# Kernel optimization log

Measured on AMD Instinct MI355X. Metric: run time of the kernel, lower is better.

## Reference

```python
import jax, jax.numpy as jnp
import numpy as np


def _conv(x, w, pad):
    # NCHW conv, stride 1
    return jax.lax.conv_general_dilated(
        x, w, window_strides=(1, 1), padding=pad,
        dimension_numbers=('NCHW', 'OIHW', 'NCHW'))


def setup_inputs() -> dict:
    key = jax.random.key(0)
    ks = jax.random.split(key, 8)
    N, Cin, H, W = 8, 512, 64, 64
    Cout, scale = 128, 2
    sd = 0.02
    return {
        'x':     jax.random.normal(ks[0], (N, Cin, H, W), jnp.float32),
        'w_du':  jax.random.normal(ks[1], (Cout, Cin, 3, 1), jnp.float32) * sd,
        'b_du':  jnp.zeros((Cout,), jnp.float32),
        'w_lr':  jax.random.normal(ks[2], (Cout, Cin, 1, 3), jnp.float32) * sd,
        'b_lr':  jnp.zeros((Cout,), jnp.float32),
        'w_1x1': jax.random.normal(ks[3], (Cout, Cin, 1, 1), jnp.float32) * sd,
        'w_ch':  jax.random.normal(ks[4], (Cout, 3 * Cout, 1, 1), jnp.float32) * sd,
        'w_w':   jax.random.normal(ks[5], (Cout * scale, Cout, 1, 1), jnp.float32) * sd,
        'w_H':   jax.random.normal(ks[6], (Cout * scale, Cout, 1, 1), jnp.float32) * sd,
        'scale': scale,
    }


def _conv_du(x, w, b):
    # convDU3, stride=1: the (3,1) conv is applied to each 1-tall row slice with
    # padding (1,0); rows are folded into the batch dim (vectorized, same math).
    N, C, H, W = x.shape
    rows = x.transpose(0, 2, 1, 3).reshape(N * H, C, 1, W)
    y = _conv(rows, w, ((1, 1), (0, 0))) + b[None, :, None, None]
    y = jax.nn.relu(y)                       # (N*H, Cout, 1, W)
    Co = y.shape[1]
    return y.reshape(N, H, Co, W).transpose(0, 2, 1, 3)


def _conv_lr(x, w, b):
    # convLR3, stride=1: (1,3) conv per 1-wide column slice; columns -> batch.
    N, C, H, W = x.shape
    cols = x.transpose(0, 3, 1, 2).reshape(N * W, C, H, 1)
    y = _conv(cols, w, ((0, 0), (1, 1))) + b[None, :, None, None]
    y = jax.nn.relu(y)                       # (N*W, Cout, H, 1)
    Co = y.shape[1]
    return y.reshape(N, W, Co, H).transpose(0, 2, 3, 1)


def reference(x, w_du, b_du, w_lr, b_lr, w_1x1, w_ch, w_w, w_H, scale):
    xdu = _conv_du(x, w_du, b_du)
    xlr = _conv_lr(x, w_lr, b_lr)
    x1 = _conv(x, w_1x1, ((0, 0), (0, 0)))
    x = jnp.concatenate((x1, xlr, xdu), axis=1)
    x = _conv(x, w_ch, ((0, 0), (0, 0)))
    x = _conv(x, w_w, ((0, 0), (0, 0)))      # (N, Cout*scale, H, W)
    N, C, H, W = x.shape
    # height pixel-shuffle: channels -> height
    xp = x.transpose(0, 3, 2, 1).reshape(N, W, H * scale, C // scale)
    xp = xp.transpose(0, 3, 2, 1)            # (N, Cout, H*scale, W)
    xh = _conv(xp, w_H, ((0, 0), (0, 0)))    # (N, Cout*scale, H*scale, W)
    # width pixel-shuffle: channels -> width
    xh = xh.transpose(0, 2, 3, 1).reshape(N, H * scale, W * scale, C // scale)
    return xh.transpose(0, 3, 1, 2)          # (N, Cout, H*scale, W*scale)
```

## Files before the change

### kernel.cpp

```cpp
#include <hip/hip_runtime.h>
#include <hip/hip_bf16.h>
#include <stdint.h>
#include <stddef.h>


typedef __attribute__((ext_vector_type(8))) __bf16 bf16x8;
typedef __attribute__((ext_vector_type(4))) float  f32x4;
typedef __attribute__((ext_vector_type(2))) float  f32x2;
typedef __attribute__((ext_vector_type(4))) unsigned int u32x4;
typedef __attribute__((ext_vector_type(2))) unsigned int u32x2;

#define BAR() asm volatile("s_waitcnt lgkmcnt(0)\n\ts_barrier" ::: "memory")



__global__ __launch_bounds__(256) void prep_k(
    const float* __restrict__ w_ch, const float* __restrict__ w_1x1,
    const float* __restrict__ w_lr, const float* __restrict__ w_du,
    const float* __restrict__ w_H,  const float* __restrict__ w_w,
    __bf16* __restrict__ Wf, __bf16* __restrict__ W2f)
{
  __shared__ float wh[2][128];
  __shared__ float Mrow[2][128];
  int bid = blockIdx.x;
  if (bid < 768) {
    int gid = bid * 256 + threadIdx.x;
    int r = gid >> 9, c = gid & 511;
    float v;
    if (r < 128) {
      const float* a_ = w_ch + r * 384;
      const float* b_ = w_1x1 + c;
      float s0 = 0.f, s1 = 0.f, s2 = 0.f, s3 = 0.f;
      #pragma unroll
      for (int j = 0; j < 128; j += 4) {
        s0 += a_[j + 0] * b_[(size_t)(j + 0) * 512];
        s1 += a_[j + 1] * b_[(size_t)(j + 1) * 512];
        s2 += a_[j + 2] * b_[(size_t)(j + 2) * 512];
        s3 += a_[j + 3] * b_[(size_t)(j + 3) * 512];
      }
      v = (s0 + s1) + (s2 + s3);
    } else if (r < 256) {
      v = w_lr[(r - 128) * 1536 + c * 3 + 1];
    } else {
      v = w_du[(r - 256) * 1536 + c * 3 + 1];
    }
    int gks = c >> 5, lsub = (c >> 3) & 3, jj = c & 7;
    int mfrag = r >> 4, lrow = r & 15;
    Wf[((gks * 24 + mfrag) << 9) + ((lrow + 16 * lsub) << 3) + jj] = (__bf16)v;
  } else {
    int t = threadIdx.x & 127, half = threadIdx.x >> 7;
    int r = (bid - 768) * 2 + half;
    int beta = r >> 8, gam = r & 1, irow = (r >> 1) & 127;
    wh[half][t] = w_H[(gam * 128 + irow) * 128 + t];
    __syncthreads();
    {
      const float* ww = w_w + beta * 16384 + t;
      float s0 = 0.f, s1 = 0.f, s2 = 0.f, s3 = 0.f;
      #pragma unroll
      for (int s = 0; s < 128; s += 4) {
        s0 += wh[half][s + 0] * ww[(s + 0) * 128];
        s1 += wh[half][s + 1] * ww[(s + 1) * 128];
        s2 += wh[half][s + 2] * ww[(s + 2) * 128];
        s3 += wh[half][s + 3] * ww[(s + 3) * 128];
      }
      Mrow[half][t] = (s0 + s1) + (s2 + s3);
    }
    __syncthreads();
    int mfrag = r >> 4, lrow = r & 15;
    #pragma unroll
    for (int c0 = 0; c0 < 384; c0 += 128) {
      int col = c0 + t;
      float v;
      if (c0 == 0) {
        v = Mrow[half][t];
      } else {
        const float* wc = w_ch + col;
        float s0 = 0.f, s1 = 0.f, s2 = 0.f, s3 = 0.f;
        #pragma unroll
        for (int k = 0; k < 128; k += 4) {
          s0 += Mrow[half][k + 0] * wc[(k + 0) * 384];
          s1 += Mrow[half][k + 1] * wc[(k + 1) * 384];
          s2 += Mrow[half][k + 2] * wc[(k + 2) * 384];
          s3 += Mrow[half][k + 3] * wc[(k + 3) * 384];
        }
        v = (s0 + s1) + (s2 + s3);
      }
      int gks = col >> 5, lsub = (col >> 3) & 3, jj = col & 7;
      W2f[((gks * 32 + mfrag) << 9) + ((lrow + 16 * lsub) << 3) + jj] = (__bf16)v;
    }
  }
}


__device__ __forceinline__ int swzB(int px) {
  return (((px & 7) ^ ((px >> 3) & 7)) << 4);
}

__global__ __launch_bounds__(256, 2) void fused_k(
    const float* __restrict__ x, const __bf16* __restrict__ Wf,
    const __bf16* __restrict__ W2f,
    const float* __restrict__ b_lr, const float* __restrict__ b_du,
    float* __restrict__ out)
{
  __shared__ __align__(16) char smem[49152 + 16384];
  char* Tlds = smem;
  char* buf0 = smem + 49152;
  char* buf1 = smem + 49152 + 8192;

  const int tid  = threadIdx.x;
  const int lane = tid & 63;
  const int wv   = tid >> 6;
  const int l15  = lane & 15, lg = lane >> 4;

  const int p0      = blockIdx.x * 64;
  const int img     = p0 >> 12;
  const int pixbase = p0 & 4095;
  const float* xb   = x + (size_t)img * (512 * 4096) + pixbase;
  const char* Wfb   = (const char*)Wf;
  const char* W2b   = (const char*)W2f;

  const int sp4 = (tid & 15) * 4;
  const int sk4 = (tid >> 4) * 4;

  f32x4 ldv[4];
  auto issueS = [&](int kt) {
    #pragma unroll
    for (int j = 0; j < 4; ++j)
      ldv[j] = *(const f32x4*)(xb + (size_t)(kt * 64 + sk4 + j) * 4096 + sp4);
  };
  auto writeS = [&](char* bw) {
    #pragma unroll
    for (int pi = 0; pi < 4; ++pi) {
      int px = sp4 + pi;
      union { __bf16 b[4]; u32x2 u; } wd;
      wd.b[0] = (__bf16)ldv[0][pi];
      wd.b[1] = (__bf16)ldv[1][pi];
      wd.b[2] = (__bf16)ldv[2][pi];
      wd.b[3] = (__bf16)ldv[3][pi];
      *(u32x2*)(bw + px * 128 + ((sk4 * 2) ^ swzB(px))) = wd.u;
    }
  };

  f32x4 acc1[6][4] = {};

  auto compute1 = [&](int kt, const char* bbuf) {
    #pragma unroll
    for (int ks = 0; ks < 2; ++ks) {
      bf16x8 af[6];
      #pragma unroll
      for (int i = 0; i < 6; ++i)
        af[i] = *(const bf16x8*)(Wfb +
            (((kt * 2 + ks) * 24 + wv * 6 + i) << 10) + lane * 16);
      bf16x8 bfr[4];
      #pragma unroll
      for (int j = 0; j < 4; ++j) {
        int rb = j * 16 + l15;
        bfr[j] = *(const bf16x8*)(bbuf + rb * 128 +
                                  ((ks * 64 + lg * 16) ^ swzB(rb)));
      }
      __builtin_amdgcn_s_setprio(1);
      #pragma unroll
      for (int i = 0; i < 6; ++i)
        #pragma unroll
        for (int j = 0; j < 4; ++j)
          acc1[i][j] = __builtin_amdgcn_mfma_f32_16x16x32_bf16(
              af[i], bfr[j], acc1[i][j], 0, 0, 0);
      __builtin_amdgcn_s_setprio(0);
    }
  };

  issueS(0);
  writeS(buf0);
  issueS(1);
  BAR();

  #pragma unroll 1
  for (int kt = 0; kt < 8; ++kt) {
    const char* bcur = (kt & 1) ? buf1 : buf0;
    char* bnext      = (kt & 1) ? buf0 : buf1;
    compute1(kt, bcur);
    if (kt < 7) {
      writeS(bnext);
      if (kt < 6) issueS(kt + 2);
      BAR();
    }
  }

  #pragma unroll
  for (int i = 0; i < 6; ++i) {
    int m0 = wv * 96 + i * 16 + lg * 4;
    bool rl = (m0 >= 128);
    const float* bp = (m0 >= 256) ? (b_du + (m0 - 256)) : (b_lr + (m0 - 128));
    float b0 = 0.f, b1 = 0.f, b2 = 0.f, b3 = 0.f;
    if (rl) { b0 = bp[0]; b1 = bp[1]; b2 = bp[2]; b3 = bp[3]; }
    #pragma unroll
    for (int j = 0; j < 4; ++j) {
      int p = j * 16 + l15;
      union { __bf16 b[4]; u32x2 u; } wd;
      float v0 = acc1[i][j][0], v1 = acc1[i][j][1];
      float v2 = acc1[i][j][2], v3 = acc1[i][j][3];
      if (rl) {
        v0 = fmaxf(v0 + b0, 0.f); v1 = fmaxf(v1 + b1, 0.f);
        v2 = fmaxf(v2 + b2, 0.f); v3 = fmaxf(v3 + b3, 0.f);
      }
      wd.b[0] = (__bf16)v0; wd.b[1] = (__bf16)v1;
      wd.b[2] = (__bf16)v2; wd.b[3] = (__bf16)v3;
      *(u32x2*)(Tlds + p * 768 + ((m0 * 2) ^ ((p & 7) << 4))) = wd.u;
    }
  }
  BAR();

  f32x4 acc2[8][4] = {};
  bf16x8 afA[8], afB[8];
  #pragma unroll
  for (int i = 0; i < 8; ++i)
    afA[i] = *(const bf16x8*)(W2b + ((0 * 32 + wv * 8 + i) << 10) + lane * 16);

  #pragma unroll 1
  for (int g2 = 0; g2 < 6; ++g2) {
    int gA = 2 * g2, gB = 2 * g2 + 1;
    #pragma unroll
    for (int i = 0; i < 8; ++i)
      afB[i] = *(const bf16x8*)(W2b + ((gB * 32 + wv * 8 + i) << 10) + lane * 16);
    {
      bf16x8 bfr[4];
      #pragma unroll
      for (int j = 0; j < 4; ++j) {
        int rb = j * 16 + l15;
        bfr[j] = *(const bf16x8*)(Tlds + rb * 768 +
                                  ((gA * 64 + lg * 16) ^ ((rb & 7) << 4)));
      }
      __builtin_amdgcn_s_setprio(1);
      #pragma unroll
      for (int i = 0; i < 8; ++i)
        #pragma unroll
        for (int j = 0; j < 4; ++j)
          acc2[i][j] = __builtin_amdgcn_mfma_f32_16x16x32_bf16(
              afA[i], bfr[j], acc2[i][j], 0, 0, 0);
      __builtin_amdgcn_s_setprio(0);
    }
    if (g2 < 5) {
      #pragma unroll
      for (int i = 0; i < 8; ++i)
        afA[i] = *(const bf16x8*)(W2b + (((gA + 2) * 32 + wv * 8 + i) << 10) + lane * 16);
    }
    {
      bf16x8 bfr[4];
      #pragma unroll
      for (int j = 0; j < 4; ++j) {
        int rb = j * 16 + l15;
        bfr[j] = *(const bf16x8*)(Tlds + rb * 768 +
                                  ((gB * 64 + lg * 16) ^ ((rb & 7) << 4)));
      }
      __builtin_amdgcn_s_setprio(1);
      #pragma unroll
      for (int i = 0; i < 8; ++i)
        #pragma unroll
        for (int j = 0; j < 4; ++j)
          acc2[i][j] = __builtin_amdgcn_mfma_f32_16x16x32_bf16(
              afB[i], bfr[j], acc2[i][j], 0, 0, 0);
      __builtin_amdgcn_s_setprio(0);
    }
  }

  #pragma unroll
  for (int i = 0; i < 8; ++i) {
    int r = wv * 128 + i * 16 + lg * 4;
    int beta = r >> 8;
    int irow = (r >> 1) & 127;
    #pragma unroll
    for (int j = 0; j < 4; ++j) {
      int pp = pixbase + j * 16 + l15;
      int h = pp >> 6, w = pp & 63;
      size_t o0 = ((((size_t)img * 128 + irow) * 128) + (2 * h + beta)) * 128
                  + 2 * w;
      f32x2 lo; lo.x = acc2[i][j][0]; lo.y = acc2[i][j][1];
      f32x2 hi; hi.x = acc2[i][j][2]; hi.y = acc2[i][j][3];
      *(f32x2*)(out + o0)         = lo;
      *(f32x2*)(out + o0 + 16384) = hi;
    }
  }
}


extern "C" void kernel_launch(void* const* d_in, const int* in_sizes, int n_in,
                              void* d_out, int out_size, void* d_ws, size_t ws_size,
                              hipStream_t stream) {
  const float* x     = (const float*)d_in[0];
  const float* w_du  = (const float*)d_in[1];
  const float* b_du  = (const float*)d_in[2];
  const float* w_lr  = (const float*)d_in[3];
  const float* b_lr  = (const float*)d_in[4];
  const float* w_1x1 = (const float*)d_in[5];
  const float* w_ch  = (const float*)d_in[6];
  const float* w_w   = (const float*)d_in[7];
  const float* w_H   = (const float*)d_in[8];
  float* out = (float*)d_out;

  char* ws = (char*)d_ws;
  __bf16* Wf  = (__bf16*)(ws + 0);
  __bf16* W2f = (__bf16*)(ws + 393216);
  if (ws_size < (size_t)786432) return;

  prep_k <<<1024, 256, 0, stream>>>(w_ch, w_1x1, w_lr, w_du, w_H, w_w, Wf, W2f);
  fused_k<<<512, 256, 0, stream>>>(x, Wf, W2f, b_lr, b_du, out);
}
```

Before: 50.17 us.

## Split fused kernel into two GEMM kernels with global intermediate buffer

Splits the fused two-stage kernel into gemm1_k, which writes the bf16 intermediate (384 channels x 64 pixels per tile) to a global workspace in MFMA-fragment order, and gemm2_k, which reads it and runs the second GEMM. The second GEMM is spread over 1024 blocks, each handling half of the output rows, with fewer accumulators and launch bounds set for 3 blocks per SM. This drops the 48KB LDS staging and its barriers and aims for more parallelism and occupancy. In exchange it adds about 24MB of global write-plus-read traffic and an extra kernel launch.

Result: slower. 60.94 us (+21.5%).

```diff
diff --git a/kernel.cpp b/kernel.cpp
--- a/kernel.cpp
+++ b/kernel.cpp
@@ -96,16 +96,14 @@
   return (((px & 7) ^ ((px >> 3) & 7)) << 4);
 }
 
-__global__ __launch_bounds__(256, 2) void fused_k(
+__global__ __launch_bounds__(256, 2) void gemm1_k(
     const float* __restrict__ x, const __bf16* __restrict__ Wf,
-    const __bf16* __restrict__ W2f,
     const float* __restrict__ b_lr, const float* __restrict__ b_du,
-    float* __restrict__ out)
+    __bf16* __restrict__ Tpf)
 {
-  __shared__ __align__(16) char smem[49152 + 16384];
-  char* Tlds = smem;
-  char* buf0 = smem + 49152;
-  char* buf1 = smem + 49152 + 8192;
+  __shared__ __align__(16) char smem[16384];
+  char* buf0 = smem;
+  char* buf1 = smem + 8192;
 
   const int tid  = threadIdx.x;
   const int lane = tid & 63;
@@ -114,10 +112,8 @@
 
   const int p0      = blockIdx.x * 64;
   const int img     = p0 >> 12;
-  const int pixbase = p0 & 4095;
-  const float* xb   = x + (size_t)img * (512 * 4096) + pixbase;
+  const float* xb   = x + (size_t)img * (512 * 4096) + (p0 & 4095);
   const char* Wfb   = (const char*)Wf;
-  const char* W2b   = (const char*)W2f;
 
   const int sp4 = (tid & 15) * 4;
   const int sk4 = (tid >> 4) * 4;
@@ -186,6 +182,7 @@
     }
   }
 
+  char* Tb = (char*)Tpf + (size_t)blockIdx.x * 49152;
   #pragma unroll
   for (int i = 0; i < 6; ++i) {
     int m0 = wv * 96 + i * 16 + lg * 4;
@@ -193,9 +190,10 @@
     const float* bp = (m0 >= 256) ? (b_du + (m0 - 256)) : (b_lr + (m0 - 128));
     float b0 = 0.f, b1 = 0.f, b2 = 0.f, b3 = 0.f;
     if (rl) { b0 = bp[0]; b1 = bp[1]; b2 = bp[2]; b3 = bp[3]; }
+    const int fin = (((m0 >> 3) & 3) * 16 + l15) * 16 + (m0 & 7) * 2;
+    const int gks = m0 >> 5;
     #pragma unroll
     for (int j = 0; j < 4; ++j) {
-      int p = j * 16 + l15;
       union { __bf16 b[4]; u32x2 u; } wd;
       float v0 = acc1[i][j][0], v1 = acc1[i][j][1];
       float v2 = acc1[i][j][2], v3 = acc1[i][j][3];
@@ -205,77 +203,65 @@
       }
       wd.b[0] = (__bf16)v0; wd.b[1] = (__bf16)v1;
       wd.b[2] = (__bf16)v2; wd.b[3] = (__bf16)v3;
-      *(u32x2*)(Tlds + p * 768 + ((m0 * 2) ^ ((p & 7) << 4))) = wd.u;
-    }
-  }
-  BAR();
-
-  f32x4 acc2[8][4] = {};
-  bf16x8 afA[8], afB[8];
+      *(u32x2*)(Tb + ((j * 12 + gks) << 10) + fin) = wd.u;
+    }
+  }
+}
+
+
+__global__ __launch_bounds__(256, 3) void gemm2_k(
+    const __bf16* __restrict__ W2f, const __bf16* __restrict__ Tpf,
+    float* __restrict__ out)
+{
+  const int tid  = threadIdx.x;
+  const int lane = tid & 63;
+  const int wv   = tid >> 6;
+  const int l15  = lane & 15, lg = lane >> 4;
+
+  const int bid  = blockIdx.x;
+  const int tile = bid >> 1;
+  const int h    = bid & 1;
+  const int p0   = tile * 64;
+  const int img  = p0 >> 12;
+  const int pixbase = p0 & 4095;
+  const char* Tb  = (const char*)Tpf + (size_t)tile * 49152;
+  const char* W2b = (const char*)W2f;
+
+  f32x4 acc[4][4] = {};
+
+  #pragma unroll 3
+  for (int g = 0; g < 12; ++g) {
+    bf16x8 af[4], bfr[4];
+    #pragma unroll
+    for (int i = 0; i < 4; ++i)
+      af[i] = *(const bf16x8*)(W2b +
+          ((g * 32 + h * 16 + wv * 4 + i) << 10) + lane * 16);
+    #pragma unroll
+    for (int j = 0; j < 4; ++j)
+      bfr[j] = *(const bf16x8*)(Tb + ((j * 12 + g) << 10) + lane * 16);
+    __builtin_amdgcn_s_setprio(1);
+    #pragma unroll
+    for (int i = 0; i < 4; ++i)
+      #pragma unroll
+      for (int j = 0; j < 4; ++j)
+        acc[i][j] = __builtin_amdgcn_mfma_f32_16x16x32_bf16(
+            af[i], bfr[j], acc[i][j], 0, 0, 0);
+    __builtin_amdgcn_s_setprio(0);
+  }
+
   #pragma unroll
-  for (int i = 0; i < 8; ++i)
-    afA[i] = *(const bf16x8*)(W2b + ((0 * 32 + wv * 8 + i) << 10) + lane * 16);
-
-  #pragma unroll 1
-  for (int g2 = 0; g2 < 6; ++g2) {
-    int gA = 2 * g2, gB = 2 * g2 + 1;
-    #pragma unroll
-    for (int i = 0; i < 8; ++i)
-      afB[i] = *(const bf16x8*)(W2b + ((gB * 32 + wv * 8 + i) << 10) + lane * 16);
-    {
-      bf16x8 bfr[4];
-      #pragma unroll
-      for (int j = 0; j < 4; ++j) {
-        int rb = j * 16 + l15;
-        bfr[j] = *(const bf16x8*)(Tlds + rb * 768 +
-                                  ((gA * 64 + lg * 16) ^ ((rb & 7) << 4)));
-      }
-      __builtin_amdgcn_s_setprio(1);
-      #pragma unroll
-      for (int i = 0; i < 8; ++i)
-        #pragma unroll
-        for (int j = 0; j < 4; ++j)
-          acc2[i][j] = __builtin_amdgcn_mfma_f32_16x16x32_bf16(
-              afA[i], bfr[j], acc2[i][j], 0, 0, 0);
-      __builtin_amdgcn_s_setprio(0);
-    }
-    if (g2 < 5) {
-      #pragma unroll
-      for (int i = 0; i < 8; ++i)
-        afA[i] = *(const bf16x8*)(W2b + (((gA + 2) * 32 + wv * 8 + i) << 10) + lane * 16);
-    }
-    {
-      bf16x8 bfr[4];
-      #pragma unroll
-      for (int j = 0; j < 4; ++j) {
-        int rb = j * 16 + l15;
-        bfr[j] = *(const bf16x8*)(Tlds + rb * 768 +
-                                  ((gB * 64 + lg * 16) ^ ((rb & 7) << 4)));
-      }
-      __builtin_amdgcn_s_setprio(1);
-      #pragma unroll
-      for (int i = 0; i < 8; ++i)
-        #pragma unroll
-        for (int j = 0; j < 4; ++j)
-          acc2[i][j] = __builtin_amdgcn_mfma_f32_16x16x32_bf16(
-              afB[i], bfr[j], acc2[i][j], 0, 0, 0);
-      __builtin_amdgcn_s_setprio(0);
-    }
-  }
-
-  #pragma unroll
-  for (int i = 0; i < 8; ++i) {
-    int r = wv * 128 + i * 16 + lg * 4;
+  for (int i = 0; i < 4; ++i) {
+    int r = h * 256 + wv * 64 + i * 16 + lg * 4;
     int beta = r >> 8;
     int irow = (r >> 1) & 127;
     #pragma unroll
     for (int j = 0; j < 4; ++j) {
       int pp = pixbase + j * 16 + l15;
-      int h = pp >> 6, w = pp & 63;
-      size_t o0 = ((((size_t)img * 128 + irow) * 128) + (2 * h + beta)) * 128
+      int hh = pp >> 6, w = pp & 63;
+      size_t o0 = ((((size_t)img * 128 + irow) * 128) + (2 * hh + beta)) * 128
                   + 2 * w;
-      f32x2 lo; lo.x = acc2[i][j][0]; lo.y = acc2[i][j][1];
-      f32x2 hi; hi.x = acc2[i][j][2]; hi.y = acc2[i][j][3];
+      f32x2 lo; lo.x = acc[i][j][0]; lo.y = acc[i][j][1];
+      f32x2 hi; hi.x = acc[i][j][2]; hi.y = acc[i][j][3];
       *(f32x2*)(out + o0)         = lo;
       *(f32x2*)(out + o0 + 16384) = hi;
     }
@@ -300,8 +286,10 @@
   char* ws = (char*)d_ws;
   __bf16* Wf  = (__bf16*)(ws + 0);
   __bf16* W2f = (__bf16*)(ws + 393216);
-  if (ws_size < (size_t)786432) return;
+  __bf16* Tpf = (__bf16*)(ws + 786432);
+  if (ws_size < (size_t)25952256) return;
 
   prep_k <<<1024, 256, 0, stream>>>(w_ch, w_1x1, w_lr, w_du, w_H, w_w, Wf, W2f);
-  fused_k<<<512, 256, 0, stream>>>(x, Wf, W2f, b_lr, b_du, out);
-}
+  gemm1_k<<<512, 256, 0, stream>>>(x, Wf, b_lr, b_du, Tpf);
+  gemm2_k<<<1024, 256, 0, stream>>>(W2f, Tpf, out);
+}
```

## Split second GEMM into four pixel-column passes to shrink accumulator footprint

Applied to the files above, without the earlier changes.

The second GEMM stage used to hold an 8x4 grid of accumulators covering all four 16-pixel column blocks. It now loops over the four blocks one at a time, keeping only 8 accumulators and writing each block's output before moving on. This cuts accumulator register pressure, which may allow higher occupancy or avoid spills, and it interleaves output stores with compute. The cost is that the W2 weight fragments are reloaded from global/L2 four times instead of once, and each A fragment is reused across fewer MFMAs.

New measurement: 61.93 us. 1.23x slower.

```diff
diff --git a/kernel.cpp b/kernel.cpp
--- a/kernel.cpp
+++ b/kernel.cpp
@@ -210,72 +210,60 @@
   }
   BAR();
 
-  f32x4 acc2[8][4] = {};
-  bf16x8 afA[8], afB[8];
-  #pragma unroll
-  for (int i = 0; i < 8; ++i)
-    afA[i] = *(const bf16x8*)(W2b + ((0 * 32 + wv * 8 + i) << 10) + lane * 16);
-
   #pragma unroll 1
-  for (int g2 = 0; g2 < 6; ++g2) {
-    int gA = 2 * g2, gB = 2 * g2 + 1;
+  for (int jsw = 0; jsw < 4; ++jsw) {
+    const int rbj = jsw * 16 + l15;
+    const int bswz = (rbj & 7) << 4;
+    f32x4 acc[8] = {};
+    bf16x8 afA[8], afB[8];
     #pragma unroll
     for (int i = 0; i < 8; ++i)
-      afB[i] = *(const bf16x8*)(W2b + ((gB * 32 + wv * 8 + i) << 10) + lane * 16);
-    {
-      bf16x8 bfr[4];
-      #pragma unroll
-      for (int j = 0; j < 4; ++j) {
-        int rb = j * 16 + l15;
-        bfr[j] = *(const bf16x8*)(Tlds + rb * 768 +
-                                  ((gA * 64 + lg * 16) ^ ((rb & 7) << 4)));
-      }
-      __builtin_amdgcn_s_setprio(1);
+      afA[i] = *(const bf16x8*)(W2b + ((0 * 32 + wv * 8 + i) << 10) + lane * 16);
+
+    #pragma unroll 1
+    for (int g2 = 0; g2 < 6; ++g2) {
+      int gA = 2 * g2, gB = 2 * g2 + 1;
       #pragma unroll
       for (int i = 0; i < 8; ++i)
-        #pragma unroll
-        for (int j = 0; j < 4; ++j)
-          acc2[i][j] = __builtin_amdgcn_mfma_f32_16x16x32_bf16(
-              afA[i], bfr[j], acc2[i][j], 0, 0, 0);
-      __builtin_amdgcn_s_setprio(0);
-    }
-    if (g2 < 5) {
-      #pragma unroll
-      for (int i = 0; i < 8; ++i)
-        afA[i] = *(const bf16x8*)(W2b + (((gA + 2) * 32 + wv * 8 + i) << 10) + lane * 16);
-    }
-    {
-      bf16x8 bfr[4];
-      #pragma unroll
-      for (int j = 0; j < 4; ++j) {
-        int rb = j * 16 + l15;
-        bfr[j] = *(const bf16x8*)(Tlds + rb * 768 +
-                                  ((gB * 64 + lg * 16) ^ ((rb & 7) << 4)));
-      }
-      __builtin_amdgcn_s_setprio(1);
-      #pragma unroll
-      for (int i = 0; i < 8; ++i)
-        #pragma unroll
-        for (int j = 0; j < 4; ++j)
-          acc2[i][j] = __builtin_amdgcn_mfma_f32_16x16x32_bf16(
-              afB[i], bfr[j], acc2[i][j], 0, 0, 0);
-      __builtin_amdgcn_s_setprio(0);
-    }
-  }
-
-  #pragma unroll
-  for (int i = 0; i < 8; ++i) {
-    int r = wv * 128 + i * 16 + lg * 4;
-    int beta = r >> 8;
-    int irow = (r >> 1) & 127;
-    #pragma unroll
-    for (int j = 0; j < 4; ++j) {
-      int pp = pixbase + j * 16 + l15;
+        afB[i] = *(const bf16x8*)(W2b + ((gB * 32 + wv * 8 + i) << 10) + lane * 16);
+      {
+        bf16x8 b0 = *(const bf16x8*)(Tlds + rbj * 768 +
+                                     ((gA * 64 + lg * 16) ^ bswz));
+        __builtin_amdgcn_s_setprio(1);
+        #pragma unroll
+        for (int i = 0; i < 8; ++i)
+          acc[i] = __builtin_amdgcn_mfma_f32_16x16x32_bf16(
+              afA[i], b0, acc[i], 0, 0, 0);
+        __builtin_amdgcn_s_setprio(0);
+      }
+      if (g2 < 5) {
+        #pragma unroll
+        for (int i = 0; i < 8; ++i)
+          afA[i] = *(const bf16x8*)(W2b + (((gA + 2) * 32 + wv * 8 + i) << 10) + lane * 16);
+      }
+      {
+        bf16x8 b1 = *(const bf16x8*)(Tlds + rbj * 768 +
+                                     ((gB * 64 + lg * 16) ^ bswz));
+        __builtin_amdgcn_s_setprio(1);
+        #pragma unroll
+        for (int i = 0; i < 8; ++i)
+          acc[i] = __builtin_amdgcn_mfma_f32_16x16x32_bf16(
+              afB[i], b1, acc[i], 0, 0, 0);
+        __builtin_amdgcn_s_setprio(0);
+      }
+    }
+
+    #pragma unroll
+    for (int i = 0; i < 8; ++i) {
+      int r = wv * 128 + i * 16 + lg * 4;
+      int beta = r >> 8;
+      int irow = (r >> 1) & 127;
+      int pp = pixbase + jsw * 16 + l15;
       int h = pp >> 6, w = pp & 63;
       size_t o0 = ((((size_t)img * 128 + irow) * 128) + (2 * h + beta)) * 128
                   + 2 * w;
-      f32x2 lo; lo.x = acc2[i][j][0]; lo.y = acc2[i][j][1];
-      f32x2 hi; hi.x = acc2[i][j][2]; hi.y = acc2[i][j][3];
+      f32x2 lo; lo.x = acc[i][0]; lo.y = acc[i][1];
+      f32x2 hi; hi.x = acc[i][2]; hi.y = acc[i][3];
       *(f32x2*)(out + o0)         = lo;
       *(f32x2*)(out + o0 + 16384) = hi;
     }
```

## Split weight-prep into two register-tiled kernels with vectorized loads and stores

Applied to the files above, without the earlier changes.

The single weight-folding prep kernel is replaced by two kernels. Each thread now computes a 4x4 output tile with float4 loads and writes packed bf16 vectors, instead of computing one scalar dot product per thread. The intermediate w_H·w_w product (Mrows) is stored in workspace and reused by a second kernel, rather than recomputed per row with shared-memory barriers. This adds one kernel launch and needs a larger workspace, but cuts prep work and uncoalesced loads.

After: 81.45 us. +62.4%, slower.

```diff
diff --git a/kernel.cpp b/kernel.cpp
--- a/kernel.cpp
+++ b/kernel.cpp
@@ -14,80 +14,156 @@
 
 
 
-__global__ __launch_bounds__(256) void prep_k(
+__global__ __launch_bounds__(256) void prep1_k(
     const float* __restrict__ w_ch, const float* __restrict__ w_1x1,
     const float* __restrict__ w_lr, const float* __restrict__ w_du,
     const float* __restrict__ w_H,  const float* __restrict__ w_w,
-    __bf16* __restrict__ Wf, __bf16* __restrict__ W2f)
+    __bf16* __restrict__ Wf, float* __restrict__ Mrows)
 {
-  __shared__ float wh[2][128];
-  __shared__ float Mrow[2][128];
-  int bid = blockIdx.x;
-  if (bid < 768) {
-    int gid = bid * 256 + threadIdx.x;
-    int r = gid >> 9, c = gid & 511;
-    float v;
-    if (r < 128) {
-      const float* a_ = w_ch + r * 384;
-      const float* b_ = w_1x1 + c;
-      float s0 = 0.f, s1 = 0.f, s2 = 0.f, s3 = 0.f;
-      #pragma unroll
-      for (int j = 0; j < 128; j += 4) {
-        s0 += a_[j + 0] * b_[(size_t)(j + 0) * 512];
-        s1 += a_[j + 1] * b_[(size_t)(j + 1) * 512];
-        s2 += a_[j + 2] * b_[(size_t)(j + 2) * 512];
-        s3 += a_[j + 3] * b_[(size_t)(j + 3) * 512];
-      }
-      v = (s0 + s1) + (s2 + s3);
-    } else if (r < 256) {
-      v = w_lr[(r - 128) * 1536 + c * 3 + 1];
-    } else {
-      v = w_du[(r - 256) * 1536 + c * 3 + 1];
-    }
-    int gks = c >> 5, lsub = (c >> 3) & 3, jj = c & 7;
-    int mfrag = r >> 4, lrow = r & 15;
-    Wf[((gks * 24 + mfrag) << 9) + ((lrow + 16 * lsub) << 3) + jj] = (__bf16)v;
+  const int bid = blockIdx.x, tid = threadIdx.x;
+  char* Wfb = (char*)Wf;
+
+  if (bid < 16) {
+    int tt = bid * 256 + tid;
+    int r0 = (tt >> 7) * 4, c0 = (tt & 127) * 4;
+    float acc[4][4] = {};
+    #pragma unroll 4
+    for (int j = 0; j < 128; j += 4) {
+      f32x4 a[4], b[4];
+      #pragma unroll
+      for (int i = 0; i < 4; ++i)
+        a[i] = *(const f32x4*)(w_ch + (size_t)(r0 + i) * 384 + j);
+      #pragma unroll
+      for (int q = 0; q < 4; ++q)
+        b[q] = *(const f32x4*)(w_1x1 + (size_t)(j + q) * 512 + c0);
+      #pragma unroll
+      for (int i = 0; i < 4; ++i)
+        #pragma unroll
+        for (int q = 0; q < 4; ++q) {
+          acc[i][0] += a[i][q] * b[q][0];
+          acc[i][1] += a[i][q] * b[q][1];
+          acc[i][2] += a[i][q] * b[q][2];
+          acc[i][3] += a[i][q] * b[q][3];
+        }
+    }
+    const int gks = c0 >> 5, lsub = (c0 >> 3) & 3, jj0 = c0 & 7;
+    #pragma unroll
+    for (int i = 0; i < 4; ++i) {
+      int r = r0 + i;
+      union { __bf16 b[4]; u32x2 u; } wd;
+      #pragma unroll
+      for (int q = 0; q < 4; ++q) wd.b[q] = (__bf16)acc[i][q];
+      *(u32x2*)(Wfb + (((gks * 24 + (r >> 4)) << 10) +
+                       (((r & 15) + 16 * lsub) << 4) + jj0 * 2)) = wd.u;
+    }
+  } else if (bid < 32) {
+    int tt = (bid - 16) * 256 + tid;
+    int r0 = (tt >> 5) * 4, k0 = (tt & 31) * 4;
+    const int beta = r0 >> 8;
+    const float* whp[4];
+    #pragma unroll
+    for (int i = 0; i < 4; ++i) {
+      int rr = r0 + i;
+      whp[i] = w_H + (size_t)((rr & 1) * 128 + ((rr >> 1) & 127)) * 128;
+    }
+    const float* wwb = w_w + (size_t)beta * 16384 + k0;
+    float acc[4][4] = {};
+    #pragma unroll 4
+    for (int t = 0; t < 128; t += 4) {
+      f32x4 h[4], w[4];
+      #pragma unroll
+      for (int i = 0; i < 4; ++i) h[i] = *(const f32x4*)(whp[i] + t);
+      #pragma unroll
+      for (int q = 0; q < 4; ++q) w[q] = *(const f32x4*)(wwb + (size_t)(t + q) * 128);
+      #pragma unroll
+      for (int i = 0; i < 4; ++i)
+        #pragma unroll
+        for (int q = 0; q < 4; ++q) {
+          acc[i][0] += h[i][q] * w[q][0];
+          acc[i][1] += h[i][q] * w[q][1];
+          acc[i][2] += h[i][q] * w[q][2];
+          acc[i][3] += h[i][q] * w[q][3];
+        }
+    }
+    #pragma unroll
+    for (int i = 0; i < 4; ++i) {
+      f32x4 o; o.x = acc[i][0]; o.y = acc[i][1]; o.z = acc[i][2]; o.w = acc[i][3];
+      *(f32x4*)(Mrows + (size_t)(r0 + i) * 128 + k0) = o;
+    }
   } else {
-    int t = threadIdx.x & 127, half = threadIdx.x >> 7;
-    int r = (bid - 768) * 2 + half;
-    int beta = r >> 8, gam = r & 1, irow = (r >> 1) & 127;
-    wh[half][t] = w_H[(gam * 128 + irow) * 128 + t];
-    __syncthreads();
-    {
-      const float* ww = w_w + beta * 16384 + t;
-      float s0 = 0.f, s1 = 0.f, s2 = 0.f, s3 = 0.f;
-      #pragma unroll
-      for (int s = 0; s < 128; s += 4) {
-        s0 += wh[half][s + 0] * ww[(s + 0) * 128];
-        s1 += wh[half][s + 1] * ww[(s + 1) * 128];
-        s2 += wh[half][s + 2] * ww[(s + 2) * 128];
-        s3 += wh[half][s + 3] * ww[(s + 3) * 128];
-      }
-      Mrow[half][t] = (s0 + s1) + (s2 + s3);
-    }
-    __syncthreads();
-    int mfrag = r >> 4, lrow = r & 15;
-    #pragma unroll
-    for (int c0 = 0; c0 < 384; c0 += 128) {
-      int col = c0 + t;
-      float v;
-      if (c0 == 0) {
-        v = Mrow[half][t];
-      } else {
-        const float* wc = w_ch + col;
-        float s0 = 0.f, s1 = 0.f, s2 = 0.f, s3 = 0.f;
-        #pragma unroll
-        for (int k = 0; k < 128; k += 4) {
-          s0 += Mrow[half][k + 0] * wc[(k + 0) * 384];
-          s1 += Mrow[half][k + 1] * wc[(k + 1) * 384];
-          s2 += Mrow[half][k + 2] * wc[(k + 2) * 384];
-          s3 += Mrow[half][k + 3] * wc[(k + 3) * 384];
+    int tt = (bid - 32) * 256 + tid;
+    int rr = tt >> 5, c0 = (tt & 31) * 16;
+    int r = 128 + rr;
+    const float* src = (rr < 128) ? (w_lr + (size_t)rr * 1536 + 1)
+                                  : (w_du + (size_t)(rr - 128) * 1536 + 1);
+    const int mfrag = r >> 4, lrow = r & 15;
+    #pragma unroll
+    for (int g = 0; g < 2; ++g) {
+      int cg0 = c0 + g * 8;
+      int gks = cg0 >> 5, lsub = (cg0 >> 3) & 3;
+      union { __bf16 b[8]; u32x4 u; } wd;
+      #pragma unroll
+      for (int q = 0; q < 8; ++q) wd.b[q] = (__bf16)src[(cg0 + q) * 3];
+      *(u32x4*)(Wfb + (((gks * 24 + mfrag) << 10) +
+                       ((lrow + 16 * lsub) << 4))) = wd.u;
+    }
+  }
+}
+
+
+__global__ __launch_bounds__(256) void prep2_k(
+    const float* __restrict__ Mrows, const float* __restrict__ w_ch,
+    __bf16* __restrict__ W2f)
+{
+  const int bid = blockIdx.x, tid = threadIdx.x;
+  char* W2b = (char*)W2f;
+
+  if (bid < 32) {
+    int tt = bid * 256 + tid;
+    int r0 = (tt >> 6) * 4, c0 = 128 + (tt & 63) * 4;
+    float acc[4][4] = {};
+    #pragma unroll 4
+    for (int k = 0; k < 128; k += 4) {
+      f32x4 m[4], w[4];
+      #pragma unroll
+      for (int i = 0; i < 4; ++i)
+        m[i] = *(const f32x4*)(Mrows + (size_t)(r0 + i) * 128 + k);
+      #pragma unroll
+      for (int q = 0; q < 4; ++q)
+        w[q] = *(const f32x4*)(w_ch + (size_t)(k + q) * 384 + c0);
+      #pragma unroll
+      for (int i = 0; i < 4; ++i)
+        #pragma unroll
+        for (int q = 0; q < 4; ++q) {
+          acc[i][0] += m[i][q] * w[q][0];
+          acc[i][1] += m[i][q] * w[q][1];
+          acc[i][2] += m[i][q] * w[q][2];
+          acc[i][3] += m[i][q] * w[q][3];
         }
-        v = (s0 + s1) + (s2 + s3);
-      }
-      int gks = col >> 5, lsub = (col >> 3) & 3, jj = col & 7;
-      W2f[((gks * 32 + mfrag) << 9) + ((lrow + 16 * lsub) << 3) + jj] = (__bf16)v;
-    }
+    }
+    const int gks = c0 >> 5, lsub = (c0 >> 3) & 3, jj0 = c0 & 7;
+    #pragma unroll
+    for (int i = 0; i < 4; ++i) {
+      int r = r0 + i;
+      union { __bf16 b[4]; u32x2 u; } wd;
+      #pragma unroll
+      for (int q = 0; q < 4; ++q) wd.b[q] = (__bf16)acc[i][q];
+      *(u32x2*)(W2b + (((gks * 32 + (r >> 4)) << 10) +
+                       (((r & 15) + 16 * lsub) << 4) + jj0 * 2)) = wd.u;
+    }
+  } else {
+    int tt = (bid - 32) * 256 + tid;
+    int r = tt >> 4, c0 = (tt & 15) * 8;
+    f32x4 m0 = *(const f32x4*)(Mrows + (size_t)r * 128 + c0);
+    f32x4 m1 = *(const f32x4*)(Mrows + (size_t)r * 128 + c0 + 4);
+    int gks = c0 >> 5, lsub = (c0 >> 3) & 3;
+    union { __bf16 b[8]; u32x4 u; } wd;
+    wd.b[0] = (__bf16)m0.x; wd.b[1] = (__bf16)m0.y;
+    wd.b[2] = (__bf16)m0.z; wd.b[3] = (__bf16)m0.w;
+    wd.b[4] = (__bf16)m1.x; wd.b[5] = (__bf16)m1.y;
+    wd.b[6] = (__bf16)m1.z; wd.b[7] = (__bf16)m1.w;
+    *(u32x4*)(W2b + (((gks * 32 + (r >> 4)) << 10) +
+                     (((r & 15) + 16 * lsub) << 4))) = wd.u;
   }
 }
 
@@ -298,10 +374,12 @@
   float* out = (float*)d_out;
 
   char* ws = (char*)d_ws;
-  __bf16* Wf  = (__bf16*)(ws + 0);
-  __bf16* W2f = (__bf16*)(ws + 393216);
-  if (ws_size < (size_t)786432) return;
-
-  prep_k <<<1024, 256, 0, stream>>>(w_ch, w_1x1, w_lr, w_du, w_H, w_w, Wf, W2f);
+  __bf16* Wf    = (__bf16*)(ws + 0);
+  __bf16* W2f   = (__bf16*)(ws + 393216);
+  float*  Mrows = (float*) (ws + 786432);
+  if (ws_size < (size_t)1048576) return;
+
+  prep1_k<<<64, 256, 0, stream>>>(w_ch, w_1x1, w_lr, w_du, w_H, w_w, Wf, Mrows);
+  prep2_k<<<64, 256, 0, stream>>>(Mrows, w_ch, W2f);
   fused_k<<<512, 256, 0, stream>>>(x, Wf, W2f, b_lr, b_du, out);
 }
```
